# Kernel tuning notes

Hardware: AMD Instinct MI355X
Metric: run time of the kernel (lower is better)

The kernel has to match this reference:

```python
import jax, jax.numpy as jnp
import numpy as np

EPS = 1e-12
H = 128  # lstm_hidden_unit_num


def _ln(z, g, b):
    mu = jnp.mean(z, axis=-1, keepdims=True)
    var = jnp.mean((z - mu) ** 2, axis=-1, keepdims=True)
    return (z - mu) * jax.lax.rsqrt(var + EPS) * g + b


def _lstm(x, W, lng, lnb):
    # LayerNormBasicLSTMCell(activation=relu, forget_bias=1, no matmul bias).
    # x: [B,T,D]; W: [D+H, 4H]; lng/lnb: [5,H] (i, j, f, o, cell-state LN)
    B = x.shape[0]

    def step(carry, xt):
        c, h = carry
        z = jnp.concatenate([xt, h], axis=-1) @ W  # [B, 4H]
        i, j, f, o = jnp.split(z, 4, axis=-1)
        i = _ln(i, lng[0], lnb[0])
        j = _ln(j, lng[1], lnb[1])
        f = _ln(f, lng[2], lnb[2])
        o = _ln(o, lng[3], lnb[3])
        new_c = c * jax.nn.sigmoid(f + 1.0) + jax.nn.sigmoid(i) * jax.nn.relu(j)
        new_h = jax.nn.relu(_ln(new_c, lng[4], lnb[4])) * jax.nn.sigmoid(o)
        return (new_c, new_h), new_h

    init = (jnp.zeros((B, H), x.dtype), jnp.zeros((B, H), x.dtype))
    _, hs = jax.lax.scan(step, init, jnp.swapaxes(x, 0, 1))
    return jnp.swapaxes(hs, 0, 1)  # [B,T,H]


def _attn(out, v, Wo, bo):
    # softmax attention over time, then dense(512, relu)
    alpha = jax.nn.softmax(jnp.einsum('bth,h->bt', out, v), axis=-1)
    ctx = jnp.einsum('bt,bth->bh', alpha, out)
    return jax.nn.relu(ctx @ Wo + bo)


def setup_inputs() -> dict:
    key = jax.random.key(0)
    ks = jax.random.split(key, 12)
    B, T, V, E = 128, 46, 8150, 300
    norm_gain = 0.8
    d = {}
    d['x1'] = jax.random.normal(ks[0], (B, T, V), jnp.float32)
    d['x2'] = jax.random.normal(ks[1], (B, T, V), jnp.float32)
    d['embed1'] = jax.random.normal(ks[2], (V, E), jnp.float32) * 0.05
    d['embed2'] = jax.random.normal(ks[3], (V, E), jnp.float32) * 0.05
    d['W_lstm1'] = jax.random.normal(ks[4], (E + H, 4 * H), jnp.float32) * 0.05
    d['W_lstm2'] = jax.random.normal(ks[5], (E + H, 4 * H), jnp.float32) * 0.05
    d['lng1'] = jnp.full((5, H), norm_gain, jnp.float32)
    d['lnb1'] = jnp.zeros((5, H), jnp.float32)
    d['lng2'] = jnp.full((5, H), norm_gain, jnp.float32)
    d['lnb2'] = jnp.zeros((5, H), jnp.float32)
    d['attn_v1'] = jax.random.normal(ks[6], (H,), jnp.float32)
    d['attn_Wo1'] = jax.random.normal(ks[7], (H, 512), jnp.float32) * 0.05
    d['attn_bo1'] = jnp.zeros((512,), jnp.float32)
    d['attn_v2'] = jax.random.normal(ks[8], (H,), jnp.float32)
    d['attn_Wo2'] = jax.random.normal(ks[9], (H, 512), jnp.float32) * 0.05
    d['attn_bo2'] = jnp.zeros((512,), jnp.float32)
    d['W_h'] = jax.random.normal(ks[10], (1024, 512), jnp.float32) * 0.05
    d['b_h'] = jnp.zeros((512,), jnp.float32)
    d['W_out'] = jax.random.normal(ks[11], (512, 2), jnp.float32) * 0.05
    d['b_out'] = jnp.zeros((2,), jnp.float32)
    return d


def reference(x1, x2, embed1, embed2, W_lstm1, W_lstm2, lng1, lnb1, lng2, lnb2,
              attn_v1, attn_Wo1, attn_bo1, attn_v2, attn_Wo2, attn_bo2,
              W_h, b_h, W_out, b_out):
    e1 = jnp.einsum('btv,ve->bte', x1, embed1)  # [B,46,300]
    e2 = jnp.einsum('btv,ve->bte', x2, embed2)
    o1 = _lstm(e1, W_lstm1, lng1, lnb1)         # [B,46,128]
    o2 = _lstm(e2, W_lstm2, lng2, lnb2)
    a1 = _attn(o1, attn_v1, attn_Wo1, attn_bo1)  # [B,512]
    a2 = _attn(o2, attn_v2, attn_Wo2, attn_bo2)
    hidden = jax.nn.relu(jnp.concatenate([a1, a2], axis=1) @ W_h + b_h)
    logits = hidden @ W_out + b_out              # [B,2]
    return logits
```

## Files before the change

kernel.cpp:

```cpp
#include <hip/hip_runtime.h>
#include <math.h>

typedef short bf16x8 __attribute__((ext_vector_type(8)));
typedef float f32x4 __attribute__((ext_vector_type(4)));

__device__ __forceinline__ ushort f2bf(float f) {
    unsigned u = __float_as_uint(f);
    u = u + 0x7FFFu + ((u >> 16) & 1u);
    return (ushort)(u >> 16);
}
__device__ __forceinline__ float bf2f(ushort h) {
    return __uint_as_float(((unsigned)h) << 16);
}

#define LSTRIDE 40

__global__ __launch_bounds__(256) void trans_kernel(
    const float* __restrict__ embed, ushort* __restrict__ Et_hi,
    ushort* __restrict__ Et_lo) {
    __shared__ float tile[64][65];
    int k0 = blockIdx.x * 64;
    int n0 = blockIdx.y * 64;
    int tid = threadIdx.x;
#pragma unroll
    for (int i = 0; i < 16; i++) {
        int idx = tid + i * 256;
        int r = idx >> 6, c = idx & 63;
        int gk = k0 + r, gn = n0 + c;
        float v = (gk < 8150 && gn < 300) ? embed[(size_t)gk * 300 + gn] : 0.f;
        tile[r][c] = v;
    }
    __syncthreads();
#pragma unroll
    for (int i = 0; i < 16; i++) {
        int idx = tid + i * 256;
        int n = idx >> 6, k = idx & 63;
        float v = tile[k][n];
        ushort h = f2bf(v);
        Et_hi[(size_t)(n0 + n) * 8192 + k0 + k] = h;
        Et_lo[(size_t)(n0 + n) * 8192 + k0 + k] = f2bf(v - bf2f(h));
    }
}

__global__ __launch_bounds__(512, 4) void e_kernel(
    const float* __restrict__ X, const ushort* __restrict__ Et_hi,
    const ushort* __restrict__ Et_lo, float* __restrict__ Eo) {
    __shared__ ushort Ah[128 * LSTRIDE], Al[128 * LSTRIDE];
    __shared__ ushort Bh[160 * LSTRIDE], Bl[160 * LSTRIDE];
    int bm = blockIdx.x * 128;
    int bn = blockIdx.y * 160;
    int kc = blockIdx.z * 512;
    int tid = threadIdx.x;
    int lane = tid & 63, w = tid >> 6;
    int quad = lane >> 4, l16 = lane & 15;
    int wm = (w & 3) * 32, wn = (w >> 2) * 80;

    int mA0 = tid >> 4, kA0 = (tid & 15) * 2;
    const float* xb0 = X + (size_t)(bm + mA0) * 8150 + kA0;
    const float* xb1 = xb0 + (size_t)32 * 8150;
    const float* xb2 = xb1 + (size_t)32 * 8150;
    const float* xb3 = xb2 + (size_t)32 * 8150;
    int lA0 = mA0 * LSTRIDE + kA0;
    int nB0 = tid >> 2, segB = tid & 3;
    size_t ebOff = (size_t)(bn + nB0) * 8192 + segB * 8;
    const ushort* ebh0 = Et_hi + ebOff;
    const ushort* ebl0 = Et_lo + ebOff;
    int lB0 = nB0 * LSTRIDE + segB * 8;
    const bool bsec = (tid < 128);
    const bool guard = (kc + 512 > 8150);

    f32x4 acc[2][5];
#pragma unroll
    for (int a = 0; a < 2; a++)
#pragma unroll
        for (int b = 0; b < 5; b++) acc[a][b] = (f32x4){0.f, 0.f, 0.f, 0.f};

    float2 a0, a1, a2, a3;
    uint4 bh0, bh1, bl0, bl1;

#define LOADAB(k0)                                                            \
    do {                                                                      \
        if (!guard || ((k0) + kA0 + 1 < 8150)) {                              \
            a0 = *(const float2*)(xb0 + (k0));                                \
            a1 = *(const float2*)(xb1 + (k0));                                \
            a2 = *(const float2*)(xb2 + (k0));                                \
            a3 = *(const float2*)(xb3 + (k0));                                \
        } else {                                                              \
            a0 = make_float2(0.f, 0.f); a1 = a0; a2 = a0; a3 = a0;            \
        }                                                                     \
        bh0 = *(const uint4*)(ebh0 + (k0));                                   \
        bl0 = *(const uint4*)(ebl0 + (k0));                                   \
        if (bsec) {                                                           \
            bh1 = *(const uint4*)(ebh0 + (size_t)128 * 8192 + (k0));          \
            bl1 = *(const uint4*)(ebl0 + (size_t)128 * 8192 + (k0));          \
        }                                                                     \
    } while (0)

#define CVT1(v, H, L)                                                         \
    do { ushort hx = f2bf((v).x), hy = f2bf((v).y);                           \
         (H).x = hx; (H).y = hy;                                              \
         (L).x = f2bf((v).x - bf2f(hx)); (L).y = f2bf((v).y - bf2f(hy)); } while (0)

#define WRITEAB()                                                             \
    do {                                                                      \
        ushort2 h0, l0, h1, l1, h2, l2, h3, l3;                               \
        CVT1(a0, h0, l0); CVT1(a1, h1, l1); CVT1(a2, h2, l2); CVT1(a3, h3, l3);\
        *(ushort2*)&Ah[lA0] = h0;                 *(ushort2*)&Al[lA0] = l0;   \
        *(ushort2*)&Ah[lA0 + 32 * LSTRIDE] = h1;  *(ushort2*)&Al[lA0 + 32 * LSTRIDE] = l1; \
        *(ushort2*)&Ah[lA0 + 64 * LSTRIDE] = h2;  *(ushort2*)&Al[lA0 + 64 * LSTRIDE] = l2; \
        *(ushort2*)&Ah[lA0 + 96 * LSTRIDE] = h3;  *(ushort2*)&Al[lA0 + 96 * LSTRIDE] = l3; \
        *(uint4*)&Bh[lB0] = bh0; *(uint4*)&Bl[lB0] = bl0;                     \
        if (bsec) {                                                           \
            *(uint4*)&Bh[lB0 + 128 * LSTRIDE] = bh1;                          \
            *(uint4*)&Bl[lB0 + 128 * LSTRIDE] = bl1;                          \
        }                                                                     \
    } while (0)

    LOADAB(kc);
    WRITEAB();
    asm volatile("s_waitcnt lgkmcnt(0)" ::: "memory");
    __builtin_amdgcn_s_barrier();

    for (int step = 0; step < 16; step++) {
        if (step < 15) {
            int k0n = kc + (step + 1) * 32;
            LOADAB(k0n);
        }
        bf16x8 a_h[2], a_l[2];
#pragma unroll
        for (int mf = 0; mf < 2; mf++) {
            int row = wm + mf * 16 + l16;
            a_h[mf] = *(const bf16x8*)&Ah[row * LSTRIDE + quad * 8];
            a_l[mf] = *(const bf16x8*)&Al[row * LSTRIDE + quad * 8];
        }
        __builtin_amdgcn_s_setprio(1);
#pragma unroll
        for (int nf = 0; nf < 5; nf++) {
            int col = wn + nf * 16 + l16;
            bf16x8 b_h = *(const bf16x8*)&Bh[col * LSTRIDE + quad * 8];
            bf16x8 b_l = *(const bf16x8*)&Bl[col * LSTRIDE + quad * 8];
#pragma unroll
            for (int mf = 0; mf < 2; mf++) {
                acc[mf][nf] = __builtin_amdgcn_mfma_f32_16x16x32_bf16(a_h[mf], b_h, acc[mf][nf], 0, 0, 0);
                acc[mf][nf] = __builtin_amdgcn_mfma_f32_16x16x32_bf16(a_h[mf], b_l, acc[mf][nf], 0, 0, 0);
                acc[mf][nf] = __builtin_amdgcn_mfma_f32_16x16x32_bf16(a_l[mf], b_h, acc[mf][nf], 0, 0, 0);
            }
        }
        __builtin_amdgcn_s_setprio(0);
        asm volatile("s_waitcnt lgkmcnt(0)" ::: "memory");
        __builtin_amdgcn_s_barrier();
        if (step < 15) {
            WRITEAB();
            asm volatile("s_waitcnt lgkmcnt(0)" ::: "memory");
        }
        __builtin_amdgcn_s_barrier();
    }
#undef LOADAB
#undef CVT1
#undef WRITEAB

#pragma unroll
    for (int mf = 0; mf < 2; mf++)
#pragma unroll
        for (int nf = 0; nf < 5; nf++) {
            int row = bm + wm + mf * 16 + quad * 4;
            int col = bn + wn + nf * 16 + l16;
#pragma unroll
            for (int i = 0; i < 4; i++)
                atomicAdd(&Eo[(size_t)(row + i) * 320 + col], acc[mf][nf][i]);
        }
}

__global__ __launch_bounds__(512, 4) void ze_kernel(
    const float* __restrict__ Eo, const float* __restrict__ W,
    float* __restrict__ Zx) {
    __shared__ ushort Ah[128 * LSTRIDE], Al[128 * LSTRIDE];
    __shared__ ushort Bh[128 * LSTRIDE], Bl[128 * LSTRIDE];
    int bm = blockIdx.x * 128;
    int bn = blockIdx.y * 128;
    int tid = threadIdx.x;
    int lane = tid & 63, w = tid >> 6;
    int quad = lane >> 4, l16 = lane & 15;
    int wm = (w & 3) * 32, wn = (w >> 2) * 64;

    f32x4 acc[2][4];
#pragma unroll
    for (int a = 0; a < 2; a++)
#pragma unroll
        for (int b = 0; b < 4; b++) acc[a][b] = (f32x4){0.f, 0.f, 0.f, 0.f};

    for (int k0 = 0; k0 < 320; k0 += 32) {
#pragma unroll
        for (int r = 0; r < 2; r++) {
            int flat = tid + r * 512;
            int m = flat >> 3, kk4 = (flat & 7) * 4;
            float4 v = *(const float4*)&Eo[(size_t)(bm + m) * 320 + k0 + kk4];
            ushort4 h, l;
            h.x = f2bf(v.x); l.x = f2bf(v.x - bf2f(h.x));
            h.y = f2bf(v.y); l.y = f2bf(v.y - bf2f(h.y));
            h.z = f2bf(v.z); l.z = f2bf(v.z - bf2f(h.z));
            h.w = f2bf(v.w); l.w = f2bf(v.w - bf2f(h.w));
            *(ushort4*)&Ah[m * LSTRIDE + kk4] = h;
            *(ushort4*)&Al[m * LSTRIDE + kk4] = l;
        }
#pragma unroll
        for (int p = 0; p < 8; p++) {
            int kk = (tid >> 7) + p * 4;
            int n = tid & 127;
            int gk = k0 + kk;
            float v = (gk < 300) ? W[(size_t)gk * 512 + bn + n] : 0.f;
            ushort h = f2bf(v);
            Bh[n * LSTRIDE + kk] = h;
            Bl[n * LSTRIDE + kk] = f2bf(v - bf2f(h));
        }
        __syncthreads();
        bf16x8 a_h[2], a_l[2];
#pragma unroll
        for (int mf = 0; mf < 2; mf++) {
            int row = wm + mf * 16 + l16;
            a_h[mf] = *(const bf16x8*)&Ah[row * LSTRIDE + quad * 8];
            a_l[mf] = *(const bf16x8*)&Al[row * LSTRIDE + quad * 8];
        }
#pragma unroll
        for (int nf = 0; nf < 4; nf++) {
            int col = wn + nf * 16 + l16;
            bf16x8 b_h = *(const bf16x8*)&Bh[col * LSTRIDE + quad * 8];
            bf16x8 b_l = *(const bf16x8*)&Bl[col * LSTRIDE + quad * 8];
#pragma unroll
            for (int mf = 0; mf < 2; mf++) {
                acc[mf][nf] = __builtin_amdgcn_mfma_f32_16x16x32_bf16(a_h[mf], b_h, acc[mf][nf], 0, 0, 0);
                acc[mf][nf] = __builtin_amdgcn_mfma_f32_16x16x32_bf16(a_h[mf], b_l, acc[mf][nf], 0, 0, 0);
                acc[mf][nf] = __builtin_amdgcn_mfma_f32_16x16x32_bf16(a_l[mf], b_h, acc[mf][nf], 0, 0, 0);
            }
        }
        __syncthreads();
    }
#pragma unroll
    for (int mf = 0; mf < 2; mf++)
#pragma unroll
        for (int nf = 0; nf < 4; nf++) {
            int row = bm + wm + mf * 16 + quad * 4;
            int col = bn + wn + nf * 16 + l16;
#pragma unroll
            for (int i = 0; i < 4; i++)
                Zx[(size_t)(row + i) * 512 + col] = acc[mf][nf][i];
        }
}

#define TT 46

__device__ __forceinline__ float sigf(float x) { return 1.f / (1.f + expf(-x)); }

__global__ __launch_bounds__(256) void lstm_kernel(
    const float* __restrict__ Zx1, const float* __restrict__ Zx2,
    const float* __restrict__ W1, const float* __restrict__ W2,
    const float* __restrict__ lng1, const float* __restrict__ lnb1,
    const float* __restrict__ lng2, const float* __restrict__ lnb2,
    float* __restrict__ o1, float* __restrict__ o2) {
    int lstm = blockIdx.x >> 5;
    int r0 = (blockIdx.x & 31) * 4;
    const float* Zx = lstm ? Zx2 : Zx1;
    const float* Wh = (lstm ? W2 : W1) + 300 * 512;
    const float* g  = lstm ? lng2 : lng1;
    const float* bb = lstm ? lnb2 : lnb1;
    float* obuf = lstm ? o2 : o1;

    __shared__ __align__(16) float hs[4][128];
    __shared__ __align__(16) float cs[4][128];
    __shared__ __align__(16) float zb[4][512];
    __shared__ float mu[4][4], rs[4][4], cmu[4], crs[4];

    int tid = threadIdx.x;
    for (int i = tid; i < 512; i += 256) {
        hs[i >> 7][i & 127] = 0.f;
        cs[i >> 7][i & 127] = 0.f;
    }
    __syncthreads();

    for (int t = 0; t < TT; t++) {
        int c0 = tid * 2;
        float2 acc[4];
#pragma unroll
        for (int r = 0; r < 4; r++)
            acc[r] = *(const float2*)&Zx[((size_t)(r0 + r) * TT + t) * 512 + c0];
        for (int k = 0; k < 128; k += 4) {
            float4 h4[4];
#pragma unroll
            for (int r = 0; r < 4; r++) h4[r] = *(const float4*)&hs[r][k];
#pragma unroll
            for (int kk = 0; kk < 4; kk++) {
                float2 wv = *(const float2*)&Wh[(size_t)(k + kk) * 512 + c0];
#pragma unroll
                for (int r = 0; r < 4; r++) {
                    float hk = ((const float*)&h4[r])[kk];
                    acc[r].x = fmaf(hk, wv.x, acc[r].x);
                    acc[r].y = fmaf(hk, wv.y, acc[r].y);
                }
            }
        }
#pragma unroll
        for (int r = 0; r < 4; r++) {
            zb[r][c0] = acc[r].x;
            zb[r][c0 + 1] = acc[r].y;
        }
        __syncthreads();

        {
            int grp = tid >> 4;
            int row = grp >> 2, gate = grp & 3;
            int l = tid & 15;
            float s = 0.f, ss = 0.f;
#pragma unroll
            for (int j = 0; j < 8; j++) {
                float v = zb[row][gate * 128 + l + j * 16];
                s += v; ss += v * v;
            }
#pragma unroll
            for (int off = 1; off < 16; off <<= 1) {
                s += __shfl_xor(s, off);
                ss += __shfl_xor(ss, off);
            }
            if (l == 0) {
                float m_ = s * (1.f / 128.f);
                mu[row][gate] = m_;
                rs[row][gate] = rsqrtf(ss * (1.f / 128.f) - m_ * m_ + 1e-12f);
            }
        }
        __syncthreads();

        float ogate[2];
#pragma unroll
        for (int ii = 0; ii < 2; ii++) {
            int idx = tid + ii * 256;
            int row = idx >> 7, col = idx & 127;
            float i_g = (zb[row][col]       - mu[row][0]) * rs[row][0] * g[0 * 128 + col] + bb[0 * 128 + col];
            float j_g = (zb[row][128 + col] - mu[row][1]) * rs[row][1] * g[1 * 128 + col] + bb[1 * 128 + col];
            float f_g = (zb[row][256 + col] - mu[row][2]) * rs[row][2] * g[2 * 128 + col] + bb[2 * 128 + col];
            float o_g = (zb[row][384 + col] - mu[row][3]) * rs[row][3] * g[3 * 128 + col] + bb[3 * 128 + col];
            float nc = cs[row][col] * sigf(f_g + 1.f) + sigf(i_g) * fmaxf(j_g, 0.f);
            cs[row][col] = nc;
            ogate[ii] = o_g;
        }
        __syncthreads();

        {
            int ww = tid >> 6, l = tid & 63;
            float v0 = cs[ww][l], v1 = cs[ww][l + 64];
            float s = v0 + v1, ss = v0 * v0 + v1 * v1;
#pragma unroll
            for (int off = 1; off < 64; off <<= 1) {
                s += __shfl_xor(s, off);
                ss += __shfl_xor(ss, off);
            }
            if (l == 0) {
                float m_ = s * (1.f / 128.f);
                cmu[ww] = m_;
                crs[ww] = rsqrtf(ss * (1.f / 128.f) - m_ * m_ + 1e-12f);
            }
        }
        __syncthreads();

#pragma unroll
        for (int ii = 0; ii < 2; ii++) {
            int idx = tid + ii * 256;
            int row = idx >> 7, col = idx & 127;
            float lnc = (cs[row][col] - cmu[row]) * crs[row] * g[4 * 128 + col] + bb[4 * 128 + col];
            float hv = fmaxf(lnc, 0.f) * sigf(ogate[ii]);
            hs[row][col] = hv;
            obuf[((size_t)(r0 + row) * TT + t) * 128 + col] = hv;
        }
        __syncthreads();
    }
}

__global__ __launch_bounds__(256) void attn_kernel(
    const float* __restrict__ o1, const float* __restrict__ o2,
    const float* __restrict__ v1, const float* __restrict__ v2,
    const float* __restrict__ Wo1, const float* __restrict__ Wo2,
    const float* __restrict__ bo1, const float* __restrict__ bo2,
    float* __restrict__ acat) {
    int lstm = blockIdx.x >> 7;
    int b = blockIdx.x & 127;
    const float* o  = (lstm ? o2 : o1) + (size_t)b * TT * 128;
    const float* v  = lstm ? v2 : v1;
    const float* Wo = lstm ? Wo2 : Wo1;
    const float* bo = lstm ? bo2 : bo1;
    __shared__ float sc[64];
    __shared__ float ctx[128];
    int tid = threadIdx.x;
    if (tid < TT) {
        float s = 0.f;
        for (int h = 0; h < 128; h++) s = fmaf(o[tid * 128 + h], v[h], s);
        sc[tid] = s;
    }
    __syncthreads();
    if (tid < 64) {
        float x = (tid < TT) ? sc[tid] : -1e30f;
        float m = x;
#pragma unroll
        for (int off = 1; off < 64; off <<= 1) m = fmaxf(m, __shfl_xor(m, off));
        float e = (tid < TT) ? expf(x - m) : 0.f;
        float s = e;
#pragma unroll
        for (int off = 1; off < 64; off <<= 1) s += __shfl_xor(s, off);
        if (tid < TT) sc[tid] = e / s;
    }
    __syncthreads();
    if (tid < 128) {
        float s = 0.f;
        for (int t = 0; t < TT; t++) s = fmaf(sc[t], o[t * 128 + tid], s);
        ctx[tid] = s;
    }
    __syncthreads();
#pragma unroll
    for (int j = 0; j < 2; j++) {
        int n = tid * 2 + j;
        float s = bo[n];
        for (int h = 0; h < 128; h++) s = fmaf(ctx[h], Wo[h * 512 + n], s);
        acat[(size_t)b * 1024 + lstm * 512 + n] = fmaxf(s, 0.f);
    }
}

__global__ __launch_bounds__(256) void final_kernel(
    const float* __restrict__ acat, const float* __restrict__ Wh,
    const float* __restrict__ bh, const float* __restrict__ Wout,
    const float* __restrict__ bout, float* __restrict__ out) {
    int b = blockIdx.x;
    __shared__ float ain[1024];
    __shared__ float hid[512];
    __shared__ float red[4];
    int tid = threadIdx.x;
    for (int i = tid; i < 1024; i += 256) ain[i] = acat[(size_t)b * 1024 + i];
    __syncthreads();
#pragma unroll
    for (int j = 0; j < 2; j++) {
        int n = tid * 2 + j;
        float s = bh[n];
        for (int k = 0; k < 1024; k++) s = fmaf(ain[k], Wh[(size_t)k * 512 + n], s);
        hid[n] = fmaxf(s, 0.f);
    }
    __syncthreads();
    for (int j = 0; j < 2; j++) {
        float p = 0.f;
        for (int k = tid; k < 512; k += 256) p = fmaf(hid[k], Wout[k * 2 + j], p);
#pragma unroll
        for (int off = 1; off < 64; off <<= 1) p += __shfl_xor(p, off);
        if ((tid & 63) == 0) red[tid >> 6] = p;
        __syncthreads();
        if (tid == 0) out[b * 2 + j] = red[0] + red[1] + red[2] + red[3] + bout[j];
        __syncthreads();
    }
}

extern "C" void kernel_launch(void* const* d_in, const int* in_sizes, int n_in,
                              void* d_out, int out_size, void* d_ws, size_t ws_size,
                              hipStream_t stream) {
    const float* x1      = (const float*)d_in[0];
    const float* x2      = (const float*)d_in[1];
    const float* embed1  = (const float*)d_in[2];
    const float* embed2  = (const float*)d_in[3];
    const float* W_lstm1 = (const float*)d_in[4];
    const float* W_lstm2 = (const float*)d_in[5];
    const float* lng1    = (const float*)d_in[6];
    const float* lnb1    = (const float*)d_in[7];
    const float* lng2    = (const float*)d_in[8];
    const float* lnb2    = (const float*)d_in[9];
    const float* attn_v1 = (const float*)d_in[10];
    const float* attn_Wo1= (const float*)d_in[11];
    const float* attn_bo1= (const float*)d_in[12];
    const float* attn_v2 = (const float*)d_in[13];
    const float* attn_Wo2= (const float*)d_in[14];
    const float* attn_bo2= (const float*)d_in[15];
    const float* W_h     = (const float*)d_in[16];
    const float* b_h     = (const float*)d_in[17];
    const float* W_out   = (const float*)d_in[18];
    const float* b_out   = (const float*)d_in[19];
    float* out = (float*)d_out;

    ushort* Et_hi = (ushort*)d_ws;
    ushort* Et_lo = Et_hi + (size_t)320 * 8192;
    float* Eo  = (float*)(Et_lo + (size_t)320 * 8192);
    float* Zx1 = Eo + (size_t)5888 * 320;
    float* Zx2 = Zx1 + 3014656;
    float* o1  = Zx2 + 3014656;
    float* o2  = o1 + 753664;
    float* acat = o2 + 753664;

    hipMemsetAsync(Eo, 0, (size_t)5888 * 320 * 4, stream);
    trans_kernel<<<dim3(128, 5), 256, 0, stream>>>(embed1, Et_hi, Et_lo);
    e_kernel<<<dim3(46, 2, 16), 512, 0, stream>>>(x1, Et_hi, Et_lo, Eo);
    ze_kernel<<<dim3(46, 4), 512, 0, stream>>>(Eo, W_lstm1, Zx1);
    hipMemsetAsync(Eo, 0, (size_t)5888 * 320 * 4, stream);
    trans_kernel<<<dim3(128, 5), 256, 0, stream>>>(embed2, Et_hi, Et_lo);
    e_kernel<<<dim3(46, 2, 16), 512, 0, stream>>>(x2, Et_hi, Et_lo, Eo);
    ze_kernel<<<dim3(46, 4), 512, 0, stream>>>(Eo, W_lstm2, Zx2);

    lstm_kernel<<<64, 256, 0, stream>>>(Zx1, Zx2, W_lstm1, W_lstm2,
                                        lng1, lnb1, lng2, lnb2, o1, o2);
    attn_kernel<<<256, 256, 0, stream>>>(o1, o2, attn_v1, attn_v2,
                                         attn_Wo1, attn_Wo2, attn_bo1, attn_bo2, acat);
    final_kernel<<<128, 256, 0, stream>>>(acat, W_h, b_h, W_out, b_out, out);
}
```

Baseline: 1.132 ms.

## Restructure LSTM recurrence: 2 rows per block, one thread per gate column

The LSTM recurrence kernel now launches 128 blocks of 1024 threads, each handling 2 batch rows instead of 4, with one thread per (row, gate column). Gate layer norms are computed with wave shuffles plus a small cross-wave reduction, and the cell state stays in registers. This doubles the parallelism of the latency-bound sequential loop and reduces work per thread per step. In exchange, each recurrent weight column is re-read by more blocks and fewer threads do the cell update.

```diff
diff --git a/kernel.cpp b/kernel.cpp
--- a/kernel.cpp
+++ b/kernel.cpp
@@ -251,123 +251,93 @@
 
 __device__ __forceinline__ float sigf(float x) { return 1.f / (1.f + expf(-x)); }
 
-__global__ __launch_bounds__(256) void lstm_kernel(
+__global__ __launch_bounds__(1024) void lstm_kernel(
     const float* __restrict__ Zx1, const float* __restrict__ Zx2,
     const float* __restrict__ W1, const float* __restrict__ W2,
     const float* __restrict__ lng1, const float* __restrict__ lnb1,
     const float* __restrict__ lng2, const float* __restrict__ lnb2,
     float* __restrict__ o1, float* __restrict__ o2) {
-    int lstm = blockIdx.x >> 5;
-    int r0 = (blockIdx.x & 31) * 4;
+    int lstm = blockIdx.x >> 6;
+    int r0 = (blockIdx.x & 63) * 2;
     const float* Zx = lstm ? Zx2 : Zx1;
     const float* Wh = (lstm ? W2 : W1) + 300 * 512;
     const float* g  = lstm ? lng2 : lng1;
     const float* bb = lstm ? lnb2 : lnb1;
     float* obuf = lstm ? o2 : o1;
 
-    __shared__ __align__(16) float hs[4][128];
-    __shared__ __align__(16) float cs[4][128];
-    __shared__ __align__(16) float zb[4][512];
-    __shared__ float mu[4][4], rs[4][4], cmu[4], crs[4];
-
-    int tid = threadIdx.x;
-    for (int i = tid; i < 512; i += 256) {
-        hs[i >> 7][i & 127] = 0.f;
-        cs[i >> 7][i & 127] = 0.f;
-    }
+    __shared__ __align__(16) float hsm[2][128];
+    __shared__ float zb[2][512];
+    __shared__ float wred[16][2];
+
+    int tid = threadIdx.x;
+    int row = tid >> 9, col = tid & 511;
+    int lane = tid & 63, w = tid >> 6;
+    int cl = tid >> 7;
+
+    if (tid < 256) hsm[tid >> 7][tid & 127] = 0.f;
+    float cstate = 0.f;
+    float gain = g[col], bias = bb[col];
+    float gc = 0.f, bc = 0.f;
+    if (tid < 256) { gc = g[512 + (tid & 127)]; bc = bb[512 + (tid & 127)]; }
+    const float* Whc = Wh + col;
+    const float* zxp = Zx + (size_t)(r0 + row) * TT * 512 + col;
+    float* obp = obuf + (size_t)(r0 + (tid >> 7)) * TT * 128 + (tid & 127);
     __syncthreads();
 
     for (int t = 0; t < TT; t++) {
-        int c0 = tid * 2;
-        float2 acc[4];
-#pragma unroll
-        for (int r = 0; r < 4; r++)
-            acc[r] = *(const float2*)&Zx[((size_t)(r0 + r) * TT + t) * 512 + c0];
+        float z0 = zxp[t * 512];
+        float acc0 = 0.f, acc1 = 0.f, acc2 = 0.f, acc3 = 0.f;
+#pragma unroll
         for (int k = 0; k < 128; k += 4) {
-            float4 h4[4];
-#pragma unroll
-            for (int r = 0; r < 4; r++) h4[r] = *(const float4*)&hs[r][k];
-#pragma unroll
-            for (int kk = 0; kk < 4; kk++) {
-                float2 wv = *(const float2*)&Wh[(size_t)(k + kk) * 512 + c0];
-#pragma unroll
-                for (int r = 0; r < 4; r++) {
-                    float hk = ((const float*)&h4[r])[kk];
-                    acc[r].x = fmaf(hk, wv.x, acc[r].x);
-                    acc[r].y = fmaf(hk, wv.y, acc[r].y);
-                }
-            }
-        }
-#pragma unroll
-        for (int r = 0; r < 4; r++) {
-            zb[r][c0] = acc[r].x;
-            zb[r][c0 + 1] = acc[r].y;
-        }
-        __syncthreads();
-
-        {
-            int grp = tid >> 4;
-            int row = grp >> 2, gate = grp & 3;
-            int l = tid & 15;
-            float s = 0.f, ss = 0.f;
-#pragma unroll
-            for (int j = 0; j < 8; j++) {
-                float v = zb[row][gate * 128 + l + j * 16];
-                s += v; ss += v * v;
-            }
-#pragma unroll
-            for (int off = 1; off < 16; off <<= 1) {
-                s += __shfl_xor(s, off);
-                ss += __shfl_xor(ss, off);
-            }
-            if (l == 0) {
-                float m_ = s * (1.f / 128.f);
-                mu[row][gate] = m_;
-                rs[row][gate] = rsqrtf(ss * (1.f / 128.f) - m_ * m_ + 1e-12f);
-            }
-        }
-        __syncthreads();
-
-        float ogate[2];
-#pragma unroll
-        for (int ii = 0; ii < 2; ii++) {
-            int idx = tid + ii * 256;
-            int row = idx >> 7, col = idx & 127;
-            float i_g = (zb[row][col]       - mu[row][0]) * rs[row][0] * g[0 * 128 + col] + bb[0 * 128 + col];
-            float j_g = (zb[row][128 + col] - mu[row][1]) * rs[row][1] * g[1 * 128 + col] + bb[1 * 128 + col];
-            float f_g = (zb[row][256 + col] - mu[row][2]) * rs[row][2] * g[2 * 128 + col] + bb[2 * 128 + col];
-            float o_g = (zb[row][384 + col] - mu[row][3]) * rs[row][3] * g[3 * 128 + col] + bb[3 * 128 + col];
-            float nc = cs[row][col] * sigf(f_g + 1.f) + sigf(i_g) * fmaxf(j_g, 0.f);
-            cs[row][col] = nc;
-            ogate[ii] = o_g;
-        }
-        __syncthreads();
-
-        {
-            int ww = tid >> 6, l = tid & 63;
-            float v0 = cs[ww][l], v1 = cs[ww][l + 64];
-            float s = v0 + v1, ss = v0 * v0 + v1 * v1;
-#pragma unroll
-            for (int off = 1; off < 64; off <<= 1) {
-                s += __shfl_xor(s, off);
-                ss += __shfl_xor(ss, off);
-            }
-            if (l == 0) {
-                float m_ = s * (1.f / 128.f);
-                cmu[ww] = m_;
-                crs[ww] = rsqrtf(ss * (1.f / 128.f) - m_ * m_ + 1e-12f);
-            }
-        }
-        __syncthreads();
-
-#pragma unroll
-        for (int ii = 0; ii < 2; ii++) {
-            int idx = tid + ii * 256;
-            int row = idx >> 7, col = idx & 127;
-            float lnc = (cs[row][col] - cmu[row]) * crs[row] * g[4 * 128 + col] + bb[4 * 128 + col];
-            float hv = fmaxf(lnc, 0.f) * sigf(ogate[ii]);
-            hs[row][col] = hv;
-            obuf[((size_t)(r0 + row) * TT + t) * 128 + col] = hv;
+            float4 h4 = *(const float4*)&hsm[row][k];
+            acc0 = fmaf(h4.x, Whc[(k + 0) * 512], acc0);
+            acc1 = fmaf(h4.y, Whc[(k + 1) * 512], acc1);
+            acc2 = fmaf(h4.z, Whc[(k + 2) * 512], acc2);
+            acc3 = fmaf(h4.w, Whc[(k + 3) * 512], acc3);
+        }
+        float z = z0 + ((acc0 + acc1) + (acc2 + acc3));
+
+        float s = z, ss = z * z;
+#pragma unroll
+        for (int off = 1; off < 64; off <<= 1) {
+            s += __shfl_xor(s, off);
+            ss += __shfl_xor(ss, off);
+        }
+        if (lane == 0) { wred[w][0] = s; wred[w][1] = ss; }
+        __syncthreads();
+        float S  = wred[cl * 2][0] + wred[cl * 2 + 1][0];
+        float SS = wred[cl * 2][1] + wred[cl * 2 + 1][1];
+        float mu = S * (1.f / 128.f);
+        float rs = rsqrtf(SS * (1.f / 128.f) - mu * mu + 1e-12f);
+        zb[row][col] = (z - mu) * rs * gain + bias;
+        __syncthreads();
+
+        float nc = 0.f, og = 0.f;
+        if (tid < 256) {
+            int rr = tid >> 7, c = tid & 127;
+            float i_g = zb[rr][c], j_g = zb[rr][128 + c], f_g = zb[rr][256 + c];
+            og = zb[rr][384 + c];
+            nc = cstate * sigf(f_g + 1.f) + sigf(i_g) * fmaxf(j_g, 0.f);
+            cstate = nc;
+        }
+        float s2 = nc, ss2 = nc * nc;
+#pragma unroll
+        for (int off = 1; off < 64; off <<= 1) {
+            s2 += __shfl_xor(s2, off);
+            ss2 += __shfl_xor(ss2, off);
+        }
+        if (lane == 0 && w < 4) { wred[w][0] = s2; wred[w][1] = ss2; }
+        __syncthreads();
+        if (tid < 256) {
+            int rr = tid >> 7;
+            float S2  = wred[rr * 2][0] + wred[rr * 2 + 1][0];
+            float SS2 = wred[rr * 2][1] + wred[rr * 2 + 1][1];
+            float cmu = S2 * (1.f / 128.f);
+            float crs = rsqrtf(SS2 * (1.f / 128.f) - cmu * cmu + 1e-12f);
+            float lnc = (nc - cmu) * crs * gc + bc;
+            float hv = fmaxf(lnc, 0.f) * sigf(og);
+            hsm[rr][tid & 127] = hv;
+            obp[t * 128] = hv;
         }
         __syncthreads();
     }
@@ -495,8 +465,8 @@
     e_kernel<<<dim3(46, 2, 16), 512, 0, stream>>>(x2, Et_hi, Et_lo, Eo);
     ze_kernel<<<dim3(46, 4), 512, 0, stream>>>(Eo, W_lstm2, Zx2);
 
-    lstm_kernel<<<64, 256, 0, stream>>>(Zx1, Zx2, W_lstm1, W_lstm2,
-                                        lng1, lnb1, lng2, lnb2, o1, o2);
+    lstm_kernel<<<128, 1024, 0, stream>>>(Zx1, Zx2, W_lstm1, W_lstm2,
+                                          lng1, lnb1, lng2, lnb2, o1, o2);
     attn_kernel<<<256, 256, 0, stream>>>(o1, o2, attn_v1, attn_v2,
                                          attn_Wo1, attn_Wo2, attn_bo1, attn_bo2, acat);
     final_kernel<<<128, 256, 0, stream>>>(acat, W_h, b_h, W_out, b_out, out);
```

Measured after the change: 1.410 ms. +24.7%, slower.
